# Performance work log

Measured on AMD Instinct MI355X. Metric: run time of the kernel, lower is better.

Reference implementation:

```python
import jax, jax.numpy as jnp
import numpy as np

BINS = 64
VMIN, VMAX = 0.0, 1.0


def _calc_histogram(x):
    # x: [B, C, H, W] float
    B, C, H, W = x.shape
    x_norm = jnp.clip((x - VMIN) / (VMAX - VMIN), 0.0, 1.0)
    flat = x_norm.reshape(B * C, H * W)
    # torch.histc semantics over [0,1]: bin i = [i/BINS, (i+1)/BINS), last bin closed.
    idx = jnp.clip((flat * BINS).astype(jnp.int32), 0, BINS - 1)  # [B*C, HW]
    row_offset = (jnp.arange(B * C, dtype=jnp.int32) * BINS)[:, None]
    flat_idx = (idx + row_offset).reshape(-1)
    counts = jax.ops.segment_sum(
        jnp.ones(flat_idx.shape, dtype=x.dtype), flat_idx,
        num_segments=B * C * BINS,
    ).reshape(B * C, BINS)
    counts = counts / jnp.clip(counts.sum(axis=1, keepdims=True), 1e-8, None)
    return counts.reshape(B, C, BINS)


def reference(fake_images, real_images):
    hist_fake = _calc_histogram(fake_images)
    hist_real = _calc_histogram(real_images)
    # loss_type == 'l1'
    return jnp.abs(hist_fake - hist_real).mean()


def setup_inputs() -> dict:
    key = jax.random.key(0)
    k1, k2 = jax.random.split(key)
    shape = (32, 3, 512, 512)
    fake_images = jax.random.uniform(k1, shape, dtype=jnp.float32)
    real_images = jax.random.uniform(k2, shape, dtype=jnp.float32)
    return {"fake_images": fake_images, "real_images": real_images}
```

## Files before the change

### kernel.cpp

```cpp
#include <hip/hip_runtime.h>


#define HW        262144
#define ROWS      96
#define NBINS     64
#define BPR       8
#define CHUNK     (HW / BPR)
#define THREADS   256
#define F4_ITERS  (CHUNK / 4 / THREADS)
#define NBLOCKS   (2 * ROWS * BPR)
#define RING      8

typedef unsigned long long u64;

#define PROC4(v) do {                                                   \
    int b0 = min((int)((v).x * 64.0f), 63);                             \
    int b1 = min((int)((v).y * 64.0f), 63);                             \
    int b2 = min((int)((v).z * 64.0f), 63);                             \
    int b3 = min((int)((v).w * 64.0f), 63);                             \
    u64 m0 = 1ull << b0, m1 = 1ull << b1;                               \
    u64 m2 = 1ull << b2, m3 = 1ull << b3;                               \
    u64 s1 = m0 ^ m1, c1 = m0 & m1;                                     \
    u64 s2 = m2 ^ m3, c2 = m2 & m3;                                     \
    u64 S  = s1 ^ s2, C  = s1 & s2;                                     \
    u64 g0 = p0 & S;  p0 ^= S;                                          \
    u64 u  = c1 ^ c2, vv = c1 & c2;                                     \
    u64 s3 = u ^ C,   w  = u & C;                                       \
    u64 t3 = vv | w;                                                    \
    u64 t  = s3 ^ g0;                                                   \
    u64 g1 = (p1 & t) | (s3 & g0);  p1 ^= t;                            \
    u64 t2 = t3 ^ g1;                                                   \
    u64 g2 = (p2 & t2) | (t3 & g1); p2 ^= t2;                           \
    u64 g3 = p3 & g2; p3 ^= g2;                                         \
    u64 g4 = p4 & g3; p4 ^= g3;                                         \
    u64 g5 = p5 & g4; p5 ^= g4;                                         \
    u64 g6 = p6 & g5; p6 ^= g5;                                         \
    p7 ^= g6;                                                           \
} while (0)

#define STAGE(fk, idx) do {                                             \
    float4 cur = fk;                                                    \
    fk = q[(idx) * THREADS];                                            \
    PROC4(cur);                                                         \
    __builtin_amdgcn_sched_barrier(0);                                  \
} while (0)

__global__ __launch_bounds__(THREADS, 6)
void hist_kernel(const float* __restrict__ fake,
                 const float* __restrict__ real,
                 unsigned int* __restrict__ partial) {
    __shared__ unsigned int bhist[NBINS];

    const int tid  = threadIdx.x;
    const int lane = tid & 63;

    if (tid < NBINS) bhist[tid] = 0u;
    __syncthreads();

    const int b     = blockIdx.x;
    const int chunk = b & (BPR - 1);
    const int rowg  = b >> 3;
    const float* src = (rowg < ROWS) ? fake : real;
    const int row    = (rowg < ROWS) ? rowg : (rowg - ROWS);

    const float4* __restrict__ q =
        (const float4*)(src + (size_t)row * HW + (size_t)chunk * CHUNK) + tid;

    u64 p0 = 0, p1 = 0, p2 = 0, p3 = 0, p4 = 0, p5 = 0, p6 = 0, p7 = 0;

    float4 f0 = q[0 * THREADS];
    float4 f1 = q[1 * THREADS];
    float4 f2 = q[2 * THREADS];
    float4 f3 = q[3 * THREADS];
    float4 f4 = q[4 * THREADS];
    float4 f5 = q[5 * THREADS];
    float4 f6 = q[6 * THREADS];
    float4 f7 = q[7 * THREADS];
    __builtin_amdgcn_sched_barrier(0);

#pragma unroll 1
    for (int i = RING; i <= F4_ITERS - RING; i += RING) {
        STAGE(f0, i + 0);
        STAGE(f1, i + 1);
        STAGE(f2, i + 2);
        STAGE(f3, i + 3);
        STAGE(f4, i + 4);
        STAGE(f5, i + 5);
        STAGE(f6, i + 6);
        STAGE(f7, i + 7);
    }
    PROC4(f0); PROC4(f1); PROC4(f2); PROC4(f3);
    PROC4(f4); PROC4(f5); PROC4(f6); PROC4(f7);

    unsigned mycnt = 0;
#pragma unroll
    for (int bb = 0; bb < NBINS; ++bb) {
        unsigned ws =
              (unsigned)__popcll(__ballot((unsigned)((p0 >> bb) & 1ull)))
            + ((unsigned)__popcll(__ballot((unsigned)((p1 >> bb) & 1ull))) << 1)
            + ((unsigned)__popcll(__ballot((unsigned)((p2 >> bb) & 1ull))) << 2)
            + ((unsigned)__popcll(__ballot((unsigned)((p3 >> bb) & 1ull))) << 3)
            + ((unsigned)__popcll(__ballot((unsigned)((p4 >> bb) & 1ull))) << 4)
            + ((unsigned)__popcll(__ballot((unsigned)((p5 >> bb) & 1ull))) << 5)
            + ((unsigned)__popcll(__ballot((unsigned)((p6 >> bb) & 1ull))) << 6)
            + ((unsigned)__popcll(__ballot((unsigned)((p7 >> bb) & 1ull))) << 7);
        if (lane == bb) mycnt = ws;
    }
    atomicAdd(&bhist[lane], mycnt);
    __syncthreads();

    if (tid < NBINS)
        partial[(size_t)b * NBINS + tid] = bhist[tid];
}

__global__ __launch_bounds__(256)
void loss1_kernel(const unsigned int* __restrict__ partial,
                  unsigned int* __restrict__ blocksum) {
    const int tid = threadIdx.x;
    const int g   = blockIdx.x * 256 + tid;
    const int r   = g >> 6;
    const int bb  = g & 63;
    unsigned cf = 0, cr = 0;
#pragma unroll
    for (int c = 0; c < BPR; ++c) {
        cf += partial[((r * BPR + c) * NBINS) + bb];
        cr += partial[(((ROWS + r) * BPR + c) * NBINS) + bb];
    }
    int d = (int)cf - (int)cr;
    int a = (d < 0) ? -d : d;
#pragma unroll
    for (int off = 32; off > 0; off >>= 1)
        a += __shfl_down(a, off, 64);
    __shared__ int wsum[4];
    if ((tid & 63) == 0) wsum[tid >> 6] = a;
    __syncthreads();
    if (tid == 0)
        blocksum[blockIdx.x] = (unsigned)(wsum[0] + wsum[1] + wsum[2] + wsum[3]);
}

__global__ __launch_bounds__(64)
void loss2_kernel(const unsigned int* __restrict__ blocksum,
                  float* __restrict__ out) {
    const int lane = threadIdx.x;
    int a = (lane < 24) ? (int)blocksum[lane] : 0;
#pragma unroll
    for (int off = 32; off > 0; off >>= 1)
        a += __shfl_down(a, off, 64);
    if (lane == 0)
        out[0] = (float)((double)a / (262144.0 * 6144.0));
}

extern "C" void kernel_launch(void* const* d_in, const int* in_sizes, int n_in,
                              void* d_out, int out_size, void* d_ws, size_t ws_size,
                              hipStream_t stream) {
    const float* fake = (const float*)d_in[0];
    const float* real = (const float*)d_in[1];
    unsigned int* partial  = (unsigned int*)d_ws;
    unsigned int* blocksum = partial + NBLOCKS * NBINS;
    float* out = (float*)d_out;

    hist_kernel<<<NBLOCKS, THREADS, 0, stream>>>(fake, real, partial);
    loss1_kernel<<<24, 256, 0, stream>>>(partial, blocksum);
    loss2_kernel<<<1, 64, 0, stream>>>(blocksum, out);
}
```

Before: 252.1 us.

## Stream histogram input through LDS with async global_load_lds ring buffer

Replaces the per-thread register ring of float4 loads with direct global-to-LDS asynchronous loads (global_load_lds), one 4-slot LDS ring per wave. Each wave owns a contiguous 8192-element slice and keeps three tiles in flight, waiting with explicit vmcnt counts before reading each tile back from LDS. The aim is to free VGPRs and keep more memory traffic in flight. The cost is extra LDS reads, 32KB of LDS per block, and occupancy hint lowered from 6 to 5. The LDS buffer is reused for the block histogram.

Result: faster. 224.5 us (-10.9%).

```diff
diff --git a/kernel.cpp b/kernel.cpp
--- a/kernel.cpp
+++ b/kernel.cpp
@@ -7,11 +7,17 @@
 #define BPR       8
 #define CHUNK     (HW / BPR)
 #define THREADS   256
-#define F4_ITERS  (CHUNK / 4 / THREADS)
 #define NBLOCKS   (2 * ROWS * BPR)
-#define RING      8
+
+#define WAVE_ELEMS 8192
+#define TILE_ELEMS 512
+#define NTILES     16
+#define RBUF       4
 
 typedef unsigned long long u64;
+typedef unsigned int u32;
+typedef const __attribute__((address_space(1))) u32* gas_t;
+typedef __attribute__((address_space(3))) u32* las_t;
 
 #define PROC4(v) do {                                                   \
     int b0 = min((int)((v).x * 64.0f), 63);                             \
@@ -38,24 +44,30 @@
     p7 ^= g6;                                                           \
 } while (0)
 
-#define STAGE(fk, idx) do {                                             \
-    float4 cur = fk;                                                    \
-    fk = q[(idx) * THREADS];                                            \
-    PROC4(cur);                                                         \
-    __builtin_amdgcn_sched_barrier(0);                                  \
+#define ISSUE(t) do {                                                   \
+    float* lp = lbase + ((t) & (RBUF - 1)) * TILE_ELEMS;                \
+    const float* gp = gbase + (t) * TILE_ELEMS + lane * 4;              \
+    __builtin_amdgcn_global_load_lds((gas_t)gp,        (las_t)(void*)lp,        16, 0, 0); \
+    __builtin_amdgcn_global_load_lds((gas_t)(gp + 256),(las_t)(void*)(lp + 256),16, 0, 0); \
 } while (0)
 
-__global__ __launch_bounds__(THREADS, 6)
+#define CONSUME(t) do {                                                 \
+    const float4* rp =                                                  \
+        (const float4*)(lbase + ((t) & (RBUF - 1)) * TILE_ELEMS);       \
+    float4 v0 = rp[lane];                                               \
+    float4 v1 = rp[lane + 64];                                          \
+    PROC4(v0); PROC4(v1);                                               \
+} while (0)
+
+__global__ __launch_bounds__(THREADS, 5)
 void hist_kernel(const float* __restrict__ fake,
                  const float* __restrict__ real,
                  unsigned int* __restrict__ partial) {
-    __shared__ unsigned int bhist[NBINS];
+    __shared__ __align__(16) float lds[4 * RBUF * TILE_ELEMS];
 
     const int tid  = threadIdx.x;
     const int lane = tid & 63;
-
-    if (tid < NBINS) bhist[tid] = 0u;
-    __syncthreads();
+    const int wv   = tid >> 6;
 
     const int b     = blockIdx.x;
     const int chunk = b & (BPR - 1);
@@ -63,34 +75,27 @@
     const float* src = (rowg < ROWS) ? fake : real;
     const int row    = (rowg < ROWS) ? rowg : (rowg - ROWS);
 
-    const float4* __restrict__ q =
-        (const float4*)(src + (size_t)row * HW + (size_t)chunk * CHUNK) + tid;
+    const float* gbase = src + (size_t)row * HW + (size_t)chunk * CHUNK
+                             + wv * WAVE_ELEMS;
+    float* lbase = &lds[wv * RBUF * TILE_ELEMS];
 
     u64 p0 = 0, p1 = 0, p2 = 0, p3 = 0, p4 = 0, p5 = 0, p6 = 0, p7 = 0;
 
-    float4 f0 = q[0 * THREADS];
-    float4 f1 = q[1 * THREADS];
-    float4 f2 = q[2 * THREADS];
-    float4 f3 = q[3 * THREADS];
-    float4 f4 = q[4 * THREADS];
-    float4 f5 = q[5 * THREADS];
-    float4 f6 = q[6 * THREADS];
-    float4 f7 = q[7 * THREADS];
-    __builtin_amdgcn_sched_barrier(0);
+    ISSUE(0); ISSUE(1); ISSUE(2);
 
 #pragma unroll 1
-    for (int i = RING; i <= F4_ITERS - RING; i += RING) {
-        STAGE(f0, i + 0);
-        STAGE(f1, i + 1);
-        STAGE(f2, i + 2);
-        STAGE(f3, i + 3);
-        STAGE(f4, i + 4);
-        STAGE(f5, i + 5);
-        STAGE(f6, i + 6);
-        STAGE(f7, i + 7);
+    for (int t = 0; t < NTILES - 3; ++t) {
+        __builtin_amdgcn_sched_barrier(0);
+        ISSUE(t + 3);
+        asm volatile("s_waitcnt vmcnt(6)" ::: "memory");
+        CONSUME(t);
     }
-    PROC4(f0); PROC4(f1); PROC4(f2); PROC4(f3);
-    PROC4(f4); PROC4(f5); PROC4(f6); PROC4(f7);
+    asm volatile("s_waitcnt vmcnt(4)" ::: "memory");
+    CONSUME(13);
+    asm volatile("s_waitcnt vmcnt(2)" ::: "memory");
+    CONSUME(14);
+    asm volatile("s_waitcnt vmcnt(0)" ::: "memory");
+    CONSUME(15);
 
     unsigned mycnt = 0;
 #pragma unroll
@@ -106,9 +111,13 @@
             + ((unsigned)__popcll(__ballot((unsigned)((p7 >> bb) & 1ull))) << 7);
         if (lane == bb) mycnt = ws;
     }
+
+    unsigned int* bhist = (unsigned int*)lds;
+    __syncthreads();
+    if (tid < NBINS) bhist[tid] = 0u;
+    __syncthreads();
     atomicAdd(&bhist[lane], mycnt);
     __syncthreads();
-
     if (tid < NBINS)
         partial[(size_t)b * NBINS + tid] = bhist[tid];
 }
```
